# Kernel optimization log

Measured on AMD Instinct MI355X. Metric: run time of the kernel, lower is better.

## Reference

```python
import jax, jax.numpy as jnp
import numpy as np

EPS = 1e-12


def _segment_softmax(logits, seg, n):
    # numerically stable softmax over edges grouped by destination node
    m = jax.ops.segment_max(logits, seg, num_segments=n)
    e = jnp.exp(logits - m[seg])
    s = jax.ops.segment_sum(e, seg, num_segments=n)
    return e / s[seg]


def _agnn(x, src, dst, beta, n):
    # cosine-similarity attention (PyG AGNNConv): alpha_ij = softmax_i(beta * <x_i/|x_i|, x_j/|x_j|>)
    norm = jnp.sqrt(jnp.sum(x * x, axis=-1, keepdims=True))
    xn = x / jnp.maximum(norm, EPS)
    logits = beta * jnp.sum(xn[dst] * xn[src], axis=-1)  # [E+N]
    alpha = _segment_softmax(logits, dst, n)
    return jax.ops.segment_sum(alpha[:, None] * x[src], dst, num_segments=n)


def setup_inputs() -> dict:
    key = jax.random.key(0)
    ks = jax.random.split(key, 6)
    N, E, F, H, C = 100000, 3200000, 512, 16, 7
    x = jax.random.normal(ks[0], (N, F), dtype=jnp.float32)
    edge_index = jax.random.randint(ks[1], (2, E), 0, N, dtype=jnp.int32)
    W1 = jax.random.normal(ks[2], (H, F), dtype=jnp.float32) * 0.05
    b1 = jnp.zeros((H,), jnp.float32)
    W2 = jax.random.normal(ks[3], (C, H), dtype=jnp.float32) * 0.2
    b2 = jnp.zeros((C,), jnp.float32)
    return {
        "x": x, "edge_index": edge_index,
        "W1": W1, "b1": b1,
        "beta2": jnp.ones((1,), jnp.float32),
        "beta3": jnp.ones((1,), jnp.float32),
        "beta4": jnp.ones((1,), jnp.float32),
        "W2": W2, "b2": b2,
    }


def reference(x, edge_index, W1, b1, beta2, beta3, beta4, W2, b2):
    N = x.shape[0]
    loop = jnp.arange(N, dtype=edge_index.dtype)
    src = jnp.concatenate([edge_index[0], loop])  # self-loops added by AGNNConv
    dst = jnp.concatenate([edge_index[1], loop])

    h = jax.nn.relu(x @ W1.T + b1)                 # lin1 on raw features (eval: dropout = id)
    h = _agnn(h, src, dst, jnp.float32(1.0), N)    # prop1: beta fixed at 1 (requires_grad=False)
    h = _agnn(h, src, dst, beta2[0], N)
    h = _agnn(h, src, dst, beta3[0], N)
    h = _agnn(h, src, dst, beta4[0], N)
    logits = h @ W2.T + b2
    return jax.nn.log_softmax(logits, axis=1)
```

## Files before the change

kernel.cpp:

```cpp
#include <hip/hip_runtime.h>
#include <hip/hip_fp16.h>
#include <math.h>

#define F 512
#define H 16
#define C 7
#define NB 512
#define BIN_CHUNK 4096

typedef _Float16 h2 __attribute__((ext_vector_type(2)));

__device__ __forceinline__ h2 as_h2(unsigned u) { return __builtin_bit_cast(h2, u); }
__device__ __forceinline__ unsigned as_u32(h2 v) { return __builtin_bit_cast(unsigned, v); }

__device__ __forceinline__ float dot2acc(h2 a, h2 b, float c) {
#if __has_builtin(__builtin_amdgcn_fdot2)
    return __builtin_amdgcn_fdot2(a, b, c, false);
#else
    return c + (float)a[0] * (float)b[0] + (float)a[1] * (float)b[1];
#endif
}

__global__ void zero_i32(int* p, int n) {
    int i = blockIdx.x * blockDim.x + threadIdx.x;
    if (i < n) p[i] = 0;
}

__global__ __launch_bounds__(256) void bin_edges(const int* __restrict__ ei, int E, int Etot,
                                                 int width, int cap, int* __restrict__ gcnt,
                                                 unsigned* __restrict__ binned) {
    __shared__ int cnt[NB];
    __shared__ int base[NB];
    int t = threadIdx.x;
    for (int i = t; i < NB; i += 256) cnt[i] = 0;
    __syncthreads();
    long chunk0 = (long)blockIdx.x * BIN_CHUNK;
    for (int k = 0; k < BIN_CHUNK / 256; ++k) {
        long e = chunk0 + k * 256 + t;
        if (e < Etot) {
            int dst = (e < E) ? ei[E + e] : (int)(e - E);
            atomicAdd(&cnt[dst / width], 1);
        }
    }
    __syncthreads();
    for (int i = t; i < NB; i += 256) {
        int c = cnt[i];
        base[i] = c ? atomicAdd(&gcnt[i], c) : 0;
        cnt[i] = 0;
    }
    __syncthreads();
    for (int k = 0; k < BIN_CHUNK / 256; ++k) {
        long e = chunk0 + k * 256 + t;
        if (e < Etot) {
            int src, dst;
            if (e < E) { src = ei[e]; dst = ei[E + e]; }
            else       { src = (int)(e - E); dst = src; }
            int b = dst / width;
            size_t pos = (size_t)b * cap + base[b] + atomicAdd(&cnt[b], 1);
            binned[pos] = (unsigned)src | ((unsigned)(dst - b * width) << 17);
        }
    }
}

__global__ void bucket_scan(const int* __restrict__ gcnt, int Etot,
                            int* __restrict__ bbase, int* __restrict__ rp, int N) {
    __shared__ int s[NB];
    int t = threadIdx.x;
    int own = gcnt[t];
    s[t] = own;
    __syncthreads();
    for (int d = 1; d < NB; d <<= 1) {
        int add = (t >= d) ? s[t - d] : 0;
        __syncthreads();
        s[t] += add;
        __syncthreads();
    }
    bbase[t] = s[t] - own;
    if (t == NB - 1) bbase[NB] = s[t];
    if (t == 0) rp[N] = Etot;
}

__global__ __launch_bounds__(256) void bucket_sort(const unsigned* __restrict__ binned,
                                                   const int* __restrict__ gcnt,
                                                   const int* __restrict__ bbase,
                                                   int width, int cap, int N,
                                                   int* __restrict__ rp, int* __restrict__ srcs) {
    __shared__ int cnt[256];
    __shared__ int cur[256];
    int b = blockIdx.x, t = threadIdx.x;
    int r0 = bbase[b];
    int ne = gcnt[b];
    const unsigned* bin = binned + (size_t)b * cap;
    int nodeBase = b * width;
    cnt[t] = 0;
    cur[t] = 0;
    __syncthreads();
    for (int e = t; e < ne; e += 256) {
        atomicAdd(&cnt[bin[e] >> 17], 1);
    }
    __syncthreads();
    int own = cnt[t];
    for (int d = 1; d < 256; d <<= 1) {
        int add = (t >= d) ? cnt[t - d] : 0;
        __syncthreads();
        cnt[t] += add;
        __syncthreads();
    }
    int excl = cnt[t] - own;
    int node = nodeBase + t;
    if (t < width && node < N) rp[node] = r0 + excl;
    __syncthreads();
    cnt[t] = excl;
    __syncthreads();
    for (int e = t; e < ne; e += 256) {
        unsigned p = bin[e];
        int dL = p >> 17;
        int pos = r0 + cnt[dL] + atomicAdd(&cur[dL], 1);
        srcs[pos] = (int)(p & 0x1FFFFu);
    }
}

__global__ __launch_bounds__(256) void lin1_relu(const float* __restrict__ x,
                                                 const float* __restrict__ W1,
                                                 const float* __restrict__ b1,
                                                 __half* __restrict__ hrow, int N) {
    __shared__ float4 w4[16 * 16 * 9];
    int t = threadIdx.x;
    for (int r = 0; r < 8; ++r) {
        int idx = r * 256 + t;
        int j = idx >> 7;
        int rem = idx & 127;
        int s = rem >> 3, m = rem & 7;
        w4[(j * 16 + s) * 9 + m] = ((const float4*)W1)[idx];
    }
    __syncthreads();

    int s = t & 15, g = t >> 4;
    int iA = blockIdx.x * 32 + g;
    int iB = iA + 16;
    int iAc = min(iA, N - 1), iBc = min(iB, N - 1);

    const float4* xA4 = (const float4*)(x + (size_t)iAc * F);
    const float4* xB4 = (const float4*)(x + (size_t)iBc * F);
    float4 xa[8], xb[8];
#pragma unroll
    for (int m = 0; m < 8; ++m) xa[m] = xA4[s * 8 + m];
#pragma unroll
    for (int m = 0; m < 8; ++m) xb[m] = xB4[s * 8 + m];

    float vA[16], vB[16];
#pragma unroll
    for (int j = 0; j < 16; ++j) { vA[j] = 0.f; vB[j] = 0.f; }
#pragma unroll
    for (int j = 0; j < 16; ++j) {
        const float4* wr = &w4[(j * 16 + s) * 9];
#pragma unroll
        for (int m = 0; m < 8; ++m) {
            float4 w = wr[m];
            vA[j] += w.x * xa[m].x + w.y * xa[m].y + w.z * xa[m].z + w.w * xa[m].w;
            vB[j] += w.x * xb[m].x + w.y * xb[m].y + w.z * xb[m].z + w.w * xb[m].w;
        }
    }

#pragma unroll
    for (int st = 0; st < 4; ++st) {
        int bit = (s >> st) & 1;
        int cntj = 16 >> (st + 1);
#pragma unroll
        for (int k = 0; k < 8; ++k) {
            if (k < cntj) {
                float keepA = bit ? vA[2 * k + 1] : vA[2 * k];
                float giveA = bit ? vA[2 * k] : vA[2 * k + 1];
                vA[k] = keepA + __shfl_xor(giveA, 1 << st);
                float keepB = bit ? vB[2 * k + 1] : vB[2 * k];
                float giveB = bit ? vB[2 * k] : vB[2 * k + 1];
                vB[k] = keepB + __shfl_xor(giveB, 1 << st);
            }
        }
    }

    float bs = b1[s];
    float oA = fmaxf(vA[0] + bs, 0.f);
    float oB = fmaxf(vB[0] + bs, 0.f);

    float sqA = oA * oA, sqB = oB * oB;
    sqA += __shfl_xor(sqA, 1); sqA += __shfl_xor(sqA, 2);
    sqA += __shfl_xor(sqA, 4); sqA += __shfl_xor(sqA, 8);
    sqB += __shfl_xor(sqB, 1); sqB += __shfl_xor(sqB, 2);
    sqB += __shfl_xor(sqB, 4); sqB += __shfl_xor(sqB, 8);
    float rnA = 1.0f / fmaxf(sqrtf(sqA), 1e-12f);
    float rnB = 1.0f / fmaxf(sqrtf(sqB), 1e-12f);

    if (iA < N) {
        hrow[(size_t)iA * 32 + s] = __float2half(oA * rnA);
        hrow[(size_t)iA * 32 + 16 + s] = __float2half(oA);
    }
    if (iB < N) {
        hrow[(size_t)iB * 32 + s] = __float2half(oB * rnB);
        hrow[(size_t)iB * 32 + 16 + s] = __float2half(oB);
    }
}

__global__ __launch_bounds__(64) void agnn_step(const uint4* __restrict__ hrow,
                                                const int* __restrict__ rp,
                                                const int* __restrict__ srcs,
                                                const float* __restrict__ bp,
                                                uint4* __restrict__ hrow_out, int N) {
    int i = blockIdx.x * 64 + threadIdx.x;
    if (i >= N) return;

    const float L2E = 1.4426950408889634f;
    float beta = bp ? bp[0] : 1.0f;
    float aL = beta * L2E;
    float mm = fabsf(beta) * L2E;

    uint4 hA = hrow[(size_t)i * 4 + 0];
    uint4 hB = hrow[(size_t)i * 4 + 1];
    h2 hi[8];
    hi[0] = as_h2(hA.x); hi[1] = as_h2(hA.y); hi[2] = as_h2(hA.z); hi[3] = as_h2(hA.w);
    hi[4] = as_h2(hB.x); hi[5] = as_h2(hB.y); hi[6] = as_h2(hB.z); hi[7] = as_h2(hB.w);

    int e0 = rp[i];
    int deg = rp[i + 1] - e0;
    int dm1 = deg - 1;

    int sbuf[4];
    uint4 rbuf[4][4];
#pragma unroll
    for (int u = 0; u < 4; ++u) {
        int s = srcs[e0 + min(u, dm1)];
        const uint4* r = hrow + (size_t)s * 4;
        rbuf[u][0] = r[0]; rbuf[u][1] = r[1]; rbuf[u][2] = r[2]; rbuf[u][3] = r[3];
        sbuf[u] = srcs[e0 + min(u + 4, dm1)];
    }

    float denom = 0.f;
    float acc[16];
#pragma unroll
    for (int j = 0; j < 16; ++j) acc[j] = 0.f;

    for (int k0 = 0; k0 < deg; k0 += 4) {
#pragma unroll
        for (int u = 0; u < 4; ++u) {
            int k = k0 + u;
            uint4 a = rbuf[u][0], b = rbuf[u][1], c = rbuf[u][2], d = rbuf[u][3];
            int snext = sbuf[u];
            sbuf[u] = srcs[e0 + min(k + 8, dm1)];
            const uint4* r = hrow + (size_t)snext * 4;
            rbuf[u][0] = r[0]; rbuf[u][1] = r[1]; rbuf[u][2] = r[2]; rbuf[u][3] = r[3];

            float dot = 0.f;
            dot = dot2acc(hi[0], as_h2(a.x), dot);
            dot = dot2acc(hi[1], as_h2(a.y), dot);
            dot = dot2acc(hi[2], as_h2(a.z), dot);
            dot = dot2acc(hi[3], as_h2(a.w), dot);
            dot = dot2acc(hi[4], as_h2(b.x), dot);
            dot = dot2acc(hi[5], as_h2(b.y), dot);
            dot = dot2acc(hi[6], as_h2(b.z), dot);
            dot = dot2acc(hi[7], as_h2(b.w), dot);

            float w = exp2f(fmaf(aL, dot, -mm));
            w = (k < deg) ? w : 0.f;
            denom += w;

            h2 c0 = as_h2(c.x), c1 = as_h2(c.y), c2 = as_h2(c.z), c3 = as_h2(c.w);
            h2 d0 = as_h2(d.x), d1 = as_h2(d.y), d2 = as_h2(d.z), d3 = as_h2(d.w);
            acc[0]  = fmaf(w, (float)c0[0], acc[0]);
            acc[1]  = fmaf(w, (float)c0[1], acc[1]);
            acc[2]  = fmaf(w, (float)c1[0], acc[2]);
            acc[3]  = fmaf(w, (float)c1[1], acc[3]);
            acc[4]  = fmaf(w, (float)c2[0], acc[4]);
            acc[5]  = fmaf(w, (float)c2[1], acc[5]);
            acc[6]  = fmaf(w, (float)c3[0], acc[6]);
            acc[7]  = fmaf(w, (float)c3[1], acc[7]);
            acc[8]  = fmaf(w, (float)d0[0], acc[8]);
            acc[9]  = fmaf(w, (float)d0[1], acc[9]);
            acc[10] = fmaf(w, (float)d1[0], acc[10]);
            acc[11] = fmaf(w, (float)d1[1], acc[11]);
            acc[12] = fmaf(w, (float)d2[0], acc[12]);
            acc[13] = fmaf(w, (float)d2[1], acc[13]);
            acc[14] = fmaf(w, (float)d3[0], acc[14]);
            acc[15] = fmaf(w, (float)d3[1], acc[15]);
        }
    }

    float rd = 1.0f / denom;
    float o[16];
    float sq = 0.f;
#pragma unroll
    for (int j = 0; j < 16; ++j) {
        o[j] = acc[j] * rd;
        sq = fmaf(o[j], o[j], sq);
    }
    float rno = 1.0f / fmaxf(sqrtf(sq), 1e-12f);

    uint4 w0, w1, w2, w3;
    {
        h2 t0, t1;
        t0[0] = (_Float16)(o[0] * rno);  t0[1] = (_Float16)(o[1] * rno);
        t1[0] = (_Float16)(o[2] * rno);  t1[1] = (_Float16)(o[3] * rno);
        w0.x = as_u32(t0); w0.y = as_u32(t1);
        t0[0] = (_Float16)(o[4] * rno);  t0[1] = (_Float16)(o[5] * rno);
        t1[0] = (_Float16)(o[6] * rno);  t1[1] = (_Float16)(o[7] * rno);
        w0.z = as_u32(t0); w0.w = as_u32(t1);
        t0[0] = (_Float16)(o[8] * rno);  t0[1] = (_Float16)(o[9] * rno);
        t1[0] = (_Float16)(o[10] * rno); t1[1] = (_Float16)(o[11] * rno);
        w1.x = as_u32(t0); w1.y = as_u32(t1);
        t0[0] = (_Float16)(o[12] * rno); t0[1] = (_Float16)(o[13] * rno);
        t1[0] = (_Float16)(o[14] * rno); t1[1] = (_Float16)(o[15] * rno);
        w1.z = as_u32(t0); w1.w = as_u32(t1);
        t0[0] = (_Float16)o[0];  t0[1] = (_Float16)o[1];
        t1[0] = (_Float16)o[2];  t1[1] = (_Float16)o[3];
        w2.x = as_u32(t0); w2.y = as_u32(t1);
        t0[0] = (_Float16)o[4];  t0[1] = (_Float16)o[5];
        t1[0] = (_Float16)o[6];  t1[1] = (_Float16)o[7];
        w2.z = as_u32(t0); w2.w = as_u32(t1);
        t0[0] = (_Float16)o[8];  t0[1] = (_Float16)o[9];
        t1[0] = (_Float16)o[10]; t1[1] = (_Float16)o[11];
        w3.x = as_u32(t0); w3.y = as_u32(t1);
        t0[0] = (_Float16)o[12]; t0[1] = (_Float16)o[13];
        t1[0] = (_Float16)o[14]; t1[1] = (_Float16)o[15];
        w3.z = as_u32(t0); w3.w = as_u32(t1);
    }
    uint4* op = hrow_out + (size_t)i * 4;
    op[0] = w0; op[1] = w1; op[2] = w2; op[3] = w3;
}

__global__ __launch_bounds__(256) void head_kernel(const uint4* __restrict__ hrow,
                                                   const float* __restrict__ W2,
                                                   const float* __restrict__ b2,
                                                   float* __restrict__ out, int N) {
    __shared__ float w2[C * H];
    __shared__ float bb[C];
    int t = threadIdx.x;
    if (t < C * H) w2[t] = W2[t];
    if (t < C) bb[t] = b2[t];
    __syncthreads();
    int i = blockIdx.x * blockDim.x + t;
    if (i >= N) return;
    uint4 cA = hrow[(size_t)i * 4 + 2];
    uint4 cB = hrow[(size_t)i * 4 + 3];
    float hv[H];
    {
        h2 v;
        v = as_h2(cA.x); hv[0] = (float)v[0];  hv[1] = (float)v[1];
        v = as_h2(cA.y); hv[2] = (float)v[0];  hv[3] = (float)v[1];
        v = as_h2(cA.z); hv[4] = (float)v[0];  hv[5] = (float)v[1];
        v = as_h2(cA.w); hv[6] = (float)v[0];  hv[7] = (float)v[1];
        v = as_h2(cB.x); hv[8] = (float)v[0];  hv[9] = (float)v[1];
        v = as_h2(cB.y); hv[10] = (float)v[0]; hv[11] = (float)v[1];
        v = as_h2(cB.z); hv[12] = (float)v[0]; hv[13] = (float)v[1];
        v = as_h2(cB.w); hv[14] = (float)v[0]; hv[15] = (float)v[1];
    }
    float lg[C];
    float m = -1e30f;
#pragma unroll
    for (int c = 0; c < C; ++c) {
        float s = bb[c];
#pragma unroll
        for (int k = 0; k < H; ++k) s += hv[k] * w2[c * H + k];
        lg[c] = s;
        m = fmaxf(m, s);
    }
    float sum = 0.f;
#pragma unroll
    for (int c = 0; c < C; ++c) sum += expf(lg[c] - m);
    float lse = m + logf(sum);
    float* op = out + (size_t)i * C;
#pragma unroll
    for (int c = 0; c < C; ++c) op[c] = lg[c] - lse;
}

extern "C" void kernel_launch(void* const* d_in, const int* in_sizes, int n_in,
                              void* d_out, int out_size, void* d_ws, size_t ws_size,
                              hipStream_t stream) {
    const float* x     = (const float*)d_in[0];
    const int*   ei    = (const int*)d_in[1];
    const float* W1    = (const float*)d_in[2];
    const float* b1    = (const float*)d_in[3];
    const float* beta2 = (const float*)d_in[4];
    const float* beta3 = (const float*)d_in[5];
    const float* beta4 = (const float*)d_in[6];
    const float* W2    = (const float*)d_in[7];
    const float* b2    = (const float*)d_in[8];
    float* out = (float*)d_out;

    int N = in_sizes[0] / F;
    int E = in_sizes[1] / 2;
    int Etot = E + N;
    int width = (N + NB - 1) / NB;
    int cap = (Etot / NB) * 5 / 4;

    char* p = (char*)d_ws;
    uint4* hr_a = (uint4*)p; p += (size_t)N * 64;
    uint4* hr_b = (uint4*)p; p += (size_t)N * 64;
    int* rp     = (int*)p;   p += (size_t)(N + 1) * 4;
    int* srcs   = (int*)p;   p += (size_t)Etot * 4;
    int* gcnt   = (int*)p;   p += (size_t)NB * 4;
    int* bbase  = (int*)p;   p += (size_t)(NB + 1) * 4;
    p = (char*)(((size_t)p + 255) & ~(size_t)255);
    unsigned* binned = (unsigned*)p; p += (size_t)NB * cap * 4;

    zero_i32<<<(NB + 255) / 256, 256, 0, stream>>>(gcnt, NB);
    bin_edges<<<(Etot + BIN_CHUNK - 1) / BIN_CHUNK, 256, 0, stream>>>(ei, E, Etot, width, cap, gcnt, binned);
    bucket_scan<<<1, NB, 0, stream>>>(gcnt, Etot, bbase, rp, N);
    bucket_sort<<<NB, 256, 0, stream>>>(binned, gcnt, bbase, width, cap, N, rp, srcs);

    lin1_relu<<<(N + 31) / 32, 256, 0, stream>>>(x, W1, b1, (__half*)hr_a, N);

    int gs = (N + 63) / 64;
    agnn_step<<<gs, 64, 0, stream>>>(hr_a, rp, srcs, nullptr, hr_b, N);
    agnn_step<<<gs, 64, 0, stream>>>(hr_b, rp, srcs, beta2, hr_a, N);
    agnn_step<<<gs, 64, 0, stream>>>(hr_a, rp, srcs, beta3, hr_b, N);
    agnn_step<<<gs, 64, 0, stream>>>(hr_b, rp, srcs, beta4, hr_a, N);

    head_kernel<<<(N + 255) / 256, 256, 0, stream>>>(hr_a, W2, b2, out, N);
}
```

Measured before the change: 656.8 us.

## Split each node's edge loop across four lanes with shuffle reduction

```diff
diff --git a/kernel.cpp b/kernel.cpp
--- a/kernel.cpp
+++ b/kernel.cpp
@@ -201,12 +201,14 @@
     }
 }
 
-__global__ __launch_bounds__(64) void agnn_step(const uint4* __restrict__ hrow,
-                                                const int* __restrict__ rp,
-                                                const int* __restrict__ srcs,
-                                                const float* __restrict__ bp,
-                                                uint4* __restrict__ hrow_out, int N) {
-    int i = blockIdx.x * 64 + threadIdx.x;
+__global__ __launch_bounds__(256) void agnn_step(const uint4* __restrict__ hrow,
+                                                 const int* __restrict__ rp,
+                                                 const int* __restrict__ srcs,
+                                                 const float* __restrict__ bp,
+                                                 uint4* __restrict__ hrow_out, int N) {
+    int t = threadIdx.x;
+    int sub = t & 3, g = t >> 2;
+    int i = blockIdx.x * 64 + g;
     if (i >= N) return;
 
     const float L2E = 1.4426950408889634f;
@@ -223,15 +225,16 @@
     int e0 = rp[i];
     int deg = rp[i + 1] - e0;
     int dm1 = deg - 1;
+    int U = (deg + 3) >> 2;
 
     int sbuf[4];
     uint4 rbuf[4][4];
 #pragma unroll
     for (int u = 0; u < 4; ++u) {
-        int s = srcs[e0 + min(u, dm1)];
+        int s = srcs[e0 + min(sub + 4 * u, dm1)];
         const uint4* r = hrow + (size_t)s * 4;
         rbuf[u][0] = r[0]; rbuf[u][1] = r[1]; rbuf[u][2] = r[2]; rbuf[u][3] = r[3];
-        sbuf[u] = srcs[e0 + min(u + 4, dm1)];
+        sbuf[u] = srcs[e0 + min(sub + 4 * (u + 4), dm1)];
     }
 
     float denom = 0.f;
@@ -239,13 +242,14 @@
 #pragma unroll
     for (int j = 0; j < 16; ++j) acc[j] = 0.f;
 
-    for (int k0 = 0; k0 < deg; k0 += 4) {
+    for (int mb = 0; mb < U; mb += 4) {
 #pragma unroll
         for (int u = 0; u < 4; ++u) {
-            int k = k0 + u;
+            int m = mb + u;
+            int k = sub + 4 * m;
             uint4 a = rbuf[u][0], b = rbuf[u][1], c = rbuf[u][2], d = rbuf[u][3];
             int snext = sbuf[u];
-            sbuf[u] = srcs[e0 + min(k + 8, dm1)];
+            sbuf[u] = srcs[e0 + min(sub + 4 * (m + 8), dm1)];
             const uint4* r = hrow + (size_t)snext * 4;
             rbuf[u][0] = r[0]; rbuf[u][1] = r[1]; rbuf[u][2] = r[2]; rbuf[u][3] = r[3];
 
@@ -284,6 +288,14 @@
         }
     }
 
+    denom += __shfl_xor(denom, 1);
+    denom += __shfl_xor(denom, 2);
+#pragma unroll
+    for (int j = 0; j < 16; ++j) {
+        acc[j] += __shfl_xor(acc[j], 1);
+        acc[j] += __shfl_xor(acc[j], 2);
+    }
+
     float rd = 1.0f / denom;
     float o[16];
     float sq = 0.f;
@@ -294,36 +306,19 @@
     }
     float rno = 1.0f / fmaxf(sqrtf(sq), 1e-12f);
 
-    uint4 w0, w1, w2, w3;
+    float scale = (sub < 2) ? rno : 1.0f;
+    int half = (sub & 1) * 8;
+    uint4 wq;
     {
         h2 t0, t1;
-        t0[0] = (_Float16)(o[0] * rno);  t0[1] = (_Float16)(o[1] * rno);
-        t1[0] = (_Float16)(o[2] * rno);  t1[1] = (_Float16)(o[3] * rno);
-        w0.x = as_u32(t0); w0.y = as_u32(t1);
-        t0[0] = (_Float16)(o[4] * rno);  t0[1] = (_Float16)(o[5] * rno);
-        t1[0] = (_Float16)(o[6] * rno);  t1[1] = (_Float16)(o[7] * rno);
-        w0.z = as_u32(t0); w0.w = as_u32(t1);
-        t0[0] = (_Float16)(o[8] * rno);  t0[1] = (_Float16)(o[9] * rno);
-        t1[0] = (_Float16)(o[10] * rno); t1[1] = (_Float16)(o[11] * rno);
-        w1.x = as_u32(t0); w1.y = as_u32(t1);
-        t0[0] = (_Float16)(o[12] * rno); t0[1] = (_Float16)(o[13] * rno);
-        t1[0] = (_Float16)(o[14] * rno); t1[1] = (_Float16)(o[15] * rno);
-        w1.z = as_u32(t0); w1.w = as_u32(t1);
-        t0[0] = (_Float16)o[0];  t0[1] = (_Float16)o[1];
-        t1[0] = (_Float16)o[2];  t1[1] = (_Float16)o[3];
-        w2.x = as_u32(t0); w2.y = as_u32(t1);
-        t0[0] = (_Float16)o[4];  t0[1] = (_Float16)o[5];
-        t1[0] = (_Float16)o[6];  t1[1] = (_Float16)o[7];
-        w2.z = as_u32(t0); w2.w = as_u32(t1);
-        t0[0] = (_Float16)o[8];  t0[1] = (_Float16)o[9];
-        t1[0] = (_Float16)o[10]; t1[1] = (_Float16)o[11];
-        w3.x = as_u32(t0); w3.y = as_u32(t1);
-        t0[0] = (_Float16)o[12]; t0[1] = (_Float16)o[13];
-        t1[0] = (_Float16)o[14]; t1[1] = (_Float16)o[15];
-        w3.z = as_u32(t0); w3.w = as_u32(t1);
-    }
-    uint4* op = hrow_out + (size_t)i * 4;
-    op[0] = w0; op[1] = w1; op[2] = w2; op[3] = w3;
+        t0[0] = (_Float16)(o[half + 0] * scale); t0[1] = (_Float16)(o[half + 1] * scale);
+        t1[0] = (_Float16)(o[half + 2] * scale); t1[1] = (_Float16)(o[half + 3] * scale);
+        wq.x = as_u32(t0); wq.y = as_u32(t1);
+        t0[0] = (_Float16)(o[half + 4] * scale); t0[1] = (_Float16)(o[half + 5] * scale);
+        t1[0] = (_Float16)(o[half + 6] * scale); t1[1] = (_Float16)(o[half + 7] * scale);
+        wq.z = as_u32(t0); wq.w = as_u32(t1);
+    }
+    hrow_out[(size_t)i * 4 + sub] = wq;
 }
 
 __global__ __launch_bounds__(256) void head_kernel(const uint4* __restrict__ hrow,
@@ -409,10 +404,10 @@
     lin1_relu<<<(N + 31) / 32, 256, 0, stream>>>(x, W1, b1, (__half*)hr_a, N);
 
     int gs = (N + 63) / 64;
-    agnn_step<<<gs, 64, 0, stream>>>(hr_a, rp, srcs, nullptr, hr_b, N);
-    agnn_step<<<gs, 64, 0, stream>>>(hr_b, rp, srcs, beta2, hr_a, N);
-    agnn_step<<<gs, 64, 0, stream>>>(hr_a, rp, srcs, beta3, hr_b, N);
-    agnn_step<<<gs, 64, 0, stream>>>(hr_b, rp, srcs, beta4, hr_a, N);
+    agnn_step<<<gs, 256, 0, stream>>>(hr_a, rp, srcs, nullptr, hr_b, N);
+    agnn_step<<<gs, 256, 0, stream>>>(hr_b, rp, srcs, beta2, hr_a, N);
+    agnn_step<<<gs, 256, 0, stream>>>(hr_a, rp, srcs, beta3, hr_b, N);
+    agnn_step<<<gs, 256, 0, stream>>>(hr_b, rp, srcs, beta4, hr_a, N);
 
     head_kernel<<<(N + 255) / 256, 256, 0, stream>>>(hr_a, W2, b2, out, N);
 }
```

New measurement: 604.3 us. 1.09x faster.
